# Kernel optimization log

Measured on AMD Instinct MI355X. Metric: run time of the kernel, lower is better.

Reference implementation:

```python
import jax, jax.numpy as jnp
import numpy as np

B, F_IN, HID, H, S = 256, 1024, 1024, 16, 128
TEMP = float((HID // H) ** 0.5)  # 8.0


def setup_inputs() -> dict:
    key = jax.random.key(0)
    ks = jax.random.split(key, 7)
    return {
        "x": jax.random.normal(ks[0], (B, F_IN, S), dtype=jnp.float32),
        "Wq": jax.random.normal(ks[1], (HID, F_IN), dtype=jnp.float32) * (1.0 / np.sqrt(F_IN)),
        "bq": jax.random.normal(ks[2], (HID,), dtype=jnp.float32) * 0.01,
        "Wk": jax.random.normal(ks[3], (HID, F_IN), dtype=jnp.float32) * (1.0 / np.sqrt(F_IN)),
        "bk": jax.random.normal(ks[4], (HID,), dtype=jnp.float32) * 0.01,
        "Wo": jax.random.normal(ks[5], (S,), dtype=jnp.float32) * (1.0 / np.sqrt(S)),
        "bo": jax.random.normal(ks[6], (1,), dtype=jnp.float32) * 0.01,
    }


def _to_heads(t):
    # (B, F, S) -> (B, H, S, F//H), matching reshape(B,H,F/H,S).permute(0,1,3,2)
    b, f, s = t.shape
    return t.reshape(b, H, f // H, s).transpose(0, 1, 3, 2)


def reference(x, Wq, bq, Wk, bk, Wo, bo):
    # 1x1 Conv1d == per-position linear over channel dim
    q = jnp.einsum('bis,hi->bhs', x, Wq) + bq[None, :, None]
    k = jnp.einsum('bis,hi->bhs', x, Wk) + bk[None, :, None]
    qh = _to_heads(q)          # (B,H,S,HID/H)
    kh = _to_heads(k)          # (B,H,S,HID/H)
    vh = _to_heads(x)          # (B,H,S,F_IN/H)  -- v is the raw input, unprojected
    scores = jnp.einsum('bhsd,bhtd->bhst', qh, kh) / TEMP
    attn = jax.nn.softmax(scores, axis=-1)
    out = jnp.einsum('bhst,bhtd->bhsd', attn, vh)   # (B,H,S,F_IN/H)
    # _reshape_from_batches: (B,H,S,dv) -> (B, F_IN, S)
    out = out.transpose(0, 1, 3, 2).reshape(x.shape[0], F_IN, S)
    # map_o: Linear(num_users, 1) over last axis, then squeeze
    score = jnp.einsum('bfs,s->bf', out, Wo) + bo[0]
    return score
```

## Files before the change

### kernel.cpp

```cpp
#include <hip/hip_runtime.h>

#define F 1024
#define S 128
#define H 16
#define D 64
#define CK 64
#define NCHUNK 16

typedef short bf16x8 __attribute__((ext_vector_type(8)));
typedef float f32x4  __attribute__((ext_vector_type(4)));

#define XS_UNITS ((size_t)256 * NCHUNK * 1024)
#define WB_UNITS ((size_t)16 * NCHUNK * 1024)
#define WS_NEED ((XS_UNITS + WB_UNITS) * 16)

struct SmemT {
    uint4 mat[2048];
    float wpart[4][S];
    float wfin[S];
};

__device__ __forceinline__ unsigned short f2bf(float f) {
    unsigned u = __float_as_uint(f);
    u += 0x7fffu + ((u >> 16) & 1u);
    return (unsigned short)(u >> 16);
}

__device__ __forceinline__ uint4 pack8(const float* f) {
    uint4 u;
    u.x = (unsigned)f2bf(f[0]) | ((unsigned)f2bf(f[1]) << 16);
    u.y = (unsigned)f2bf(f[2]) | ((unsigned)f2bf(f[3]) << 16);
    u.z = (unsigned)f2bf(f[4]) | ((unsigned)f2bf(f[5]) << 16);
    u.w = (unsigned)f2bf(f[6]) | ((unsigned)f2bf(f[7]) << 16);
    return u;
}

typedef __attribute__((address_space(1))) const unsigned int as1_u32;
typedef __attribute__((address_space(3))) unsigned int as3_u32;

__device__ __forceinline__ void async_cp16(const uint4* g, uint4* l) {
    __builtin_amdgcn_global_load_lds((as1_u32*)g, (as3_u32*)l, 16, 0, 0);
}

__global__ void prep(const float* __restrict__ x,
                     const float* __restrict__ Wq,
                     const float* __restrict__ Wk,
                     uint4* __restrict__ xs,
                     uint4* __restrict__ wb)
{
    __shared__ float tile[64 * 129];
    const int tid = threadIdx.x;
    const int blk = blockIdx.x;
    if (blk < 4096) {
        const int b = blk >> 4, ch = blk & 15;
        const float4* src = (const float4*)(x + ((size_t)b * F + ch * CK) * S);
        float4 v[8];
#pragma unroll
        for (int j = 0; j < 8; ++j) v[j] = src[tid + j * 256];
#pragma unroll
        for (int j = 0; j < 8; ++j) {
            const int e4 = tid + j * 256;
            const int i  = e4 >> 5;
            const int sc = (e4 & 31) * 4;
            tile[i * 129 + sc + 0] = v[j].x;
            tile[i * 129 + sc + 1] = v[j].y;
            tile[i * 129 + sc + 2] = v[j].z;
            tile[i * 129 + sc + 3] = v[j].w;
        }
        __syncthreads();
#pragma unroll
        for (int j = 0; j < 4; ++j) {
            const int u   = tid + j * 256;
            const int s   = u >> 3;
            const int kc  = (u & 7) ^ (s & 7);
            float f[8];
#pragma unroll
            for (int jj = 0; jj < 8; ++jj) f[jj] = tile[(kc * 8 + jj) * 129 + s];
            xs[((size_t)(b * NCHUNK + ch)) * 1024 + u] = pack8(f);
        }
    } else {
        const int blk2 = blk - 4096;
        const int h = blk2 >> 4, ch = blk2 & 15;
#pragma unroll
        for (int j = 0; j < 4; ++j) {
            const int u   = tid + j * 256;
            const int row = u >> 3;
            const int kc  = (u & 7) ^ (row & 7);
            const float* src = (row < 64)
                ? (Wq + (size_t)(h * D + row) * F + ch * CK + kc * 8)
                : (Wk + (size_t)(h * D + row - 64) * F + ch * CK + kc * 8);
            float f[8];
            float4 a = ((const float4*)src)[0];
            float4 c = ((const float4*)src)[1];
            f[0] = a.x; f[1] = a.y; f[2] = a.z; f[3] = a.w;
            f[4] = c.x; f[5] = c.y; f[6] = c.z; f[7] = c.w;
            wb[((size_t)(h * NCHUNK + ch)) * 1024 + u] = pack8(f);
        }
    }
}

__launch_bounds__(256, 4)
__global__ void attn_main(const float* __restrict__ x,
                          const uint4* __restrict__ xs,
                          const uint4* __restrict__ wb,
                          const float* __restrict__ bq,
                          const float* __restrict__ bk,
                          const float* __restrict__ Wo,
                          const float* __restrict__ bo,
                          float* __restrict__ out)
{
    __shared__ SmemT sm;
    const int tid  = threadIdx.x;
    const int lane = tid & 63;
    const int wv   = tid >> 6;
    const int l15  = lane & 15;
    const int q    = lane >> 4;

    const int g    = blockIdx.x;
    const int xcd  = g & 7;
    const int slot = g >> 3;
    const int hg   = slot >> 7;
    const int r0   = slot & 127;
    const int b    = xcd * 32 + (r0 >> 2);
    const int h    = hg * 4 + (r0 & 3);

    const float* xb = x + (size_t)b * (F * S);
    const uint4* xc = xs + ((size_t)b * NCHUNK) * 1024;
    const uint4* wc = wb + ((size_t)h * NCHUNK) * 1024;

    const int m0 = (wv & 1) * 64;
    const int n0 = (wv >> 1) * 64;

    f32x4 acc[4][4];
#pragma unroll
    for (int mt = 0; mt < 4; ++mt)
#pragma unroll
        for (int nt = 0; nt < 4; ++nt) acc[mt][nt] = (f32x4){0.f, 0.f, 0.f, 0.f};

    for (int ch = 0; ch < NCHUNK; ++ch) {
        __syncthreads();
        const uint4* wg = wc + ch * 1024 + wv * 256;
        const uint4* xg = xc + ch * 1024 + wv * 256;
#pragma unroll
        for (int k = 0; k < 4; ++k)
            async_cp16(wg + k * 64 + lane, &sm.mat[wv * 256 + k * 64]);
#pragma unroll
        for (int k = 0; k < 4; ++k)
            async_cp16(xg + k * 64 + lane, &sm.mat[1024 + wv * 256 + k * 64]);
        __syncthreads();
#pragma unroll
        for (int ks = 0; ks < 2; ++ks) {
            bf16x8 af[4], br[4];
#pragma unroll
            for (int mt = 0; mt < 4; ++mt) {
                const int row = m0 + mt * 16 + l15;
                af[mt] = *(const bf16x8*)&sm.mat[row * 8 + ((ks * 4 + q) ^ (row & 7))];
            }
#pragma unroll
            for (int nt = 0; nt < 4; ++nt) {
                const int row = n0 + nt * 16 + l15;
                br[nt] = *(const bf16x8*)&sm.mat[1024 + row * 8 + ((ks * 4 + q) ^ (row & 7))];
            }
#pragma unroll
            for (int mt = 0; mt < 4; ++mt)
#pragma unroll
                for (int nt = 0; nt < 4; ++nt)
                    acc[mt][nt] = __builtin_amdgcn_mfma_f32_16x16x32_bf16(
                        af[mt], br[nt], acc[mt][nt], 0, 0, 0);
        }
    }

    __syncthreads();
    {
        unsigned short* m16 = (unsigned short*)sm.mat;
#pragma unroll
        for (int mt = 0; mt < 4; ++mt) {
#pragma unroll
            for (int rr = 0; rr < 4; ++rr) {
                const int m = m0 + mt * 16 + q * 4 + rr;
                const int d = m & 63;
                const float bias = (m < 64) ? bq[h * D + d] : bk[h * D + d];
                const int base = (m < 64) ? 0 : 8192;
#pragma unroll
                for (int nt = 0; nt < 4; ++nt) {
                    const int s = n0 + nt * 16 + l15;
                    const float v = acc[mt][nt][rr] + bias;
                    const int unit = s * 8 + (((d >> 3)) ^ (s & 7));
                    m16[base + unit * 8 + (d & 7)] = f2bf(v);
                }
            }
        }
    }
    __syncthreads();

    f32x4 p[2][8];
#pragma unroll
    for (int mt = 0; mt < 2; ++mt)
#pragma unroll
        for (int nt = 0; nt < 8; ++nt) p[mt][nt] = (f32x4){0.f, 0.f, 0.f, 0.f};

#pragma unroll
    for (int ks = 0; ks < 2; ++ks) {
        bf16x8 a2[2], b2[8];
#pragma unroll
        for (int mt = 0; mt < 2; ++mt) {
            const int row = wv * 32 + mt * 16 + l15;
            a2[mt] = *(const bf16x8*)&sm.mat[row * 8 + ((ks * 4 + q) ^ (row & 7))];
        }
#pragma unroll
        for (int nt = 0; nt < 8; ++nt) {
            const int row = nt * 16 + l15;
            b2[nt] = *(const bf16x8*)&sm.mat[1024 + row * 8 + ((ks * 4 + q) ^ (row & 7))];
        }
#pragma unroll
        for (int mt = 0; mt < 2; ++mt)
#pragma unroll
            for (int nt = 0; nt < 8; ++nt)
                p[mt][nt] = __builtin_amdgcn_mfma_f32_16x16x32_bf16(a2[mt], b2[nt], p[mt][nt], 0, 0, 0);
    }

    float pw[8];
#pragma unroll
    for (int nt = 0; nt < 8; ++nt) pw[nt] = 0.f;

#pragma unroll
    for (int mt = 0; mt < 2; ++mt) {
#pragma unroll
        for (int rr = 0; rr < 4; ++rr) {
            const int srow = wv * 32 + mt * 16 + q * 4 + rr;
            float mx = p[mt][0][rr];
#pragma unroll
            for (int nt = 1; nt < 8; ++nt) mx = fmaxf(mx, p[mt][nt][rr]);
#pragma unroll
            for (int off = 1; off < 16; off <<= 1) mx = fmaxf(mx, __shfl_xor(mx, off));
            float e[8];
            float l = 0.f;
#pragma unroll
            for (int nt = 0; nt < 8; ++nt) {
                e[nt] = __expf((p[mt][nt][rr] - mx) * 0.125f);
                l += e[nt];
            }
#pragma unroll
            for (int off = 1; off < 16; off <<= 1) l += __shfl_xor(l, off);
            const float c = Wo[srow] / l;
#pragma unroll
            for (int nt = 0; nt < 8; ++nt) pw[nt] = fmaf(c, e[nt], pw[nt]);
        }
    }
#pragma unroll
    for (int nt = 0; nt < 8; ++nt) {
        pw[nt] += __shfl_xor(pw[nt], 16);
        pw[nt] += __shfl_xor(pw[nt], 32);
    }
    if (q == 0) {
#pragma unroll
        for (int nt = 0; nt < 8; ++nt) sm.wpart[wv][nt * 16 + l15] = pw[nt];
    }
    __syncthreads();
    if (tid < S)
        sm.wfin[tid] = sm.wpart[0][tid] + sm.wpart[1][tid] + sm.wpart[2][tid] + sm.wpart[3][tid];
    __syncthreads();

    {
        const int dd   = tid >> 2;
        const int part = tid & 3;
        const float* xv = xb + (size_t)(h * D + dd) * S + part * 32;
        float a5 = 0.f;
#pragma unroll 8
        for (int t = 0; t < 32; ++t) a5 = fmaf(sm.wfin[part * 32 + t], xv[t], a5);
        a5 += __shfl_xor(a5, 1);
        a5 += __shfl_xor(a5, 2);
        if (part == 0) out[(size_t)b * F + h * D + dd] = a5 + bo[0];
    }
}

__launch_bounds__(256, 4)
__global__ void attn_fallback(const float* __restrict__ x,
                              const float* __restrict__ Wq,
                              const float* __restrict__ bq,
                              const float* __restrict__ Wk,
                              const float* __restrict__ bk,
                              const float* __restrict__ Wo,
                              const float* __restrict__ bo,
                              float* __restrict__ out)
{
    __shared__ SmemT sm;
    const int tid  = threadIdx.x;
    const int lane = tid & 63;
    const int wv   = tid >> 6;
    const int l15  = lane & 15;
    const int q    = lane >> 4;

    const int g    = blockIdx.x;
    const int xcd  = g & 7;
    const int slot = g >> 3;
    const int hg   = slot >> 7;
    const int r0   = slot & 127;
    const int b    = xcd * 32 + (r0 >> 2);
    const int h    = hg * 4 + (r0 & 3);

    const float* xb  = x  + (size_t)b * (F * S);
    const float* wqh = Wq + (size_t)h * D * F;
    const float* wkh = Wk + (size_t)h * D * F;

    const int m0 = (wv & 1) * 64;
    const int n0 = (wv >> 1) * 64;

    f32x4 acc[4][4];
#pragma unroll
    for (int mt = 0; mt < 4; ++mt)
#pragma unroll
        for (int nt = 0; nt < 4; ++nt) acc[mt][nt] = (f32x4){0.f, 0.f, 0.f, 0.f};

    const int mq  = tid >> 2;
    const int kq  = tid & 3;
    const int s0x = (tid & 63) * 2;
    const int iq  = tid >> 6;

    for (int ch = 0; ch < NCHUNK; ++ch) {
        const int c0 = ch * CK;
        __syncthreads();
        {
            const int key = mq & 7;
            float f[16];
            const float4* srcq = (const float4*)(wqh + (size_t)mq * F + (c0 + kq * 16));
#pragma unroll
            for (int j = 0; j < 4; ++j) {
                float4 v = srcq[j];
                f[4*j] = v.x; f[4*j+1] = v.y; f[4*j+2] = v.z; f[4*j+3] = v.w;
            }
            sm.mat[mq * 8 + ((kq * 2    ) ^ key)] = pack8(f);
            sm.mat[mq * 8 + ((kq * 2 + 1) ^ key)] = pack8(f + 8);
            const float4* srck = (const float4*)(wkh + (size_t)mq * F + (c0 + kq * 16));
#pragma unroll
            for (int j = 0; j < 4; ++j) {
                float4 v = srck[j];
                f[4*j] = v.x; f[4*j+1] = v.y; f[4*j+2] = v.z; f[4*j+3] = v.w;
            }
            sm.mat[(64 + mq) * 8 + ((kq * 2    ) ^ key)] = pack8(f);
            sm.mat[(64 + mq) * 8 + ((kq * 2 + 1) ^ key)] = pack8(f + 8);
        }
        {
            const float* src = xb + (size_t)(c0 + iq * 16) * S + s0x;
            float fa[8], fb[8];
#pragma unroll
            for (int grp = 0; grp < 2; ++grp) {
#pragma unroll
                for (int j = 0; j < 8; ++j) {
                    float2 v = *(const float2*)(src + (size_t)(grp * 8 + j) * S);
                    fa[j] = v.x; fb[j] = v.y;
                }
                const int kc = iq * 2 + grp;
                sm.mat[1024 + (s0x    ) * 8 + (kc ^ ((s0x    ) & 7))] = pack8(fa);
                sm.mat[1024 + (s0x + 1) * 8 + (kc ^ ((s0x + 1) & 7))] = pack8(fb);
            }
        }
        __syncthreads();
#pragma unroll
        for (int ks = 0; ks < 2; ++ks) {
            bf16x8 af[4], br[4];
#pragma unroll
            for (int mt = 0; mt < 4; ++mt) {
                const int row = m0 + mt * 16 + l15;
                af[mt] = *(const bf16x8*)&sm.mat[row * 8 + ((ks * 4 + q) ^ (row & 7))];
            }
#pragma unroll
            for (int nt = 0; nt < 4; ++nt) {
                const int row = n0 + nt * 16 + l15;
                br[nt] = *(const bf16x8*)&sm.mat[1024 + row * 8 + ((ks * 4 + q) ^ (row & 7))];
            }
#pragma unroll
            for (int mt = 0; mt < 4; ++mt)
#pragma unroll
                for (int nt = 0; nt < 4; ++nt)
                    acc[mt][nt] = __builtin_amdgcn_mfma_f32_16x16x32_bf16(
                        af[mt], br[nt], acc[mt][nt], 0, 0, 0);
        }
    }

    __syncthreads();
    {
        unsigned short* m16 = (unsigned short*)sm.mat;
#pragma unroll
        for (int mt = 0; mt < 4; ++mt) {
#pragma unroll
            for (int rr = 0; rr < 4; ++rr) {
                const int m = m0 + mt * 16 + q * 4 + rr;
                const int d = m & 63;
                const float bias = (m < 64) ? bq[h * D + d] : bk[h * D + d];
                const int base = (m < 64) ? 0 : 8192;
#pragma unroll
                for (int nt = 0; nt < 4; ++nt) {
                    const int s = n0 + nt * 16 + l15;
                    const float v = acc[mt][nt][rr] + bias;
                    const int unit = s * 8 + (((d >> 3)) ^ (s & 7));
                    m16[base + unit * 8 + (d & 7)] = f2bf(v);
                }
            }
        }
    }
    __syncthreads();

    f32x4 p[2][8];
#pragma unroll
    for (int mt = 0; mt < 2; ++mt)
#pragma unroll
        for (int nt = 0; nt < 8; ++nt) p[mt][nt] = (f32x4){0.f, 0.f, 0.f, 0.f};

#pragma unroll
    for (int ks = 0; ks < 2; ++ks) {
        bf16x8 a2[2], b2[8];
#pragma unroll
        for (int mt = 0; mt < 2; ++mt) {
            const int row = wv * 32 + mt * 16 + l15;
            a2[mt] = *(const bf16x8*)&sm.mat[row * 8 + ((ks * 4 + q) ^ (row & 7))];
        }
#pragma unroll
        for (int nt = 0; nt < 8; ++nt) {
            const int row = nt * 16 + l15;
            b2[nt] = *(const bf16x8*)&sm.mat[1024 + row * 8 + ((ks * 4 + q) ^ (row & 7))];
        }
#pragma unroll
        for (int mt = 0; mt < 2; ++mt)
#pragma unroll
            for (int nt = 0; nt < 8; ++nt)
                p[mt][nt] = __builtin_amdgcn_mfma_f32_16x16x32_bf16(a2[mt], b2[nt], p[mt][nt], 0, 0, 0);
    }

    float pw[8];
#pragma unroll
    for (int nt = 0; nt < 8; ++nt) pw[nt] = 0.f;

#pragma unroll
    for (int mt = 0; mt < 2; ++mt) {
#pragma unroll
        for (int rr = 0; rr < 4; ++rr) {
            const int srow = wv * 32 + mt * 16 + q * 4 + rr;
            float mx = p[mt][0][rr];
#pragma unroll
            for (int nt = 1; nt < 8; ++nt) mx = fmaxf(mx, p[mt][nt][rr]);
#pragma unroll
            for (int off = 1; off < 16; off <<= 1) mx = fmaxf(mx, __shfl_xor(mx, off));
            float e[8];
            float l = 0.f;
#pragma unroll
            for (int nt = 0; nt < 8; ++nt) {
                e[nt] = __expf((p[mt][nt][rr] - mx) * 0.125f);
                l += e[nt];
            }
#pragma unroll
            for (int off = 1; off < 16; off <<= 1) l += __shfl_xor(l, off);
            const float c = Wo[srow] / l;
#pragma unroll
            for (int nt = 0; nt < 8; ++nt) pw[nt] = fmaf(c, e[nt], pw[nt]);
        }
    }
#pragma unroll
    for (int nt = 0; nt < 8; ++nt) {
        pw[nt] += __shfl_xor(pw[nt], 16);
        pw[nt] += __shfl_xor(pw[nt], 32);
    }
    if (q == 0) {
#pragma unroll
        for (int nt = 0; nt < 8; ++nt) sm.wpart[wv][nt * 16 + l15] = pw[nt];
    }
    __syncthreads();
    if (tid < S)
        sm.wfin[tid] = sm.wpart[0][tid] + sm.wpart[1][tid] + sm.wpart[2][tid] + sm.wpart[3][tid];
    __syncthreads();

    {
        const int dd   = tid >> 2;
        const int part = tid & 3;
        const float* xv = xb + (size_t)(h * D + dd) * S + part * 32;
        float a5 = 0.f;
#pragma unroll 8
        for (int t = 0; t < 32; ++t) a5 = fmaf(sm.wfin[part * 32 + t], xv[t], a5);
        a5 += __shfl_xor(a5, 1);
        a5 += __shfl_xor(a5, 2);
        if (part == 0) out[(size_t)b * F + h * D + dd] = a5 + bo[0];
    }
}

extern "C" void kernel_launch(void* const* d_in, const int* in_sizes, int n_in,
                              void* d_out, int out_size, void* d_ws, size_t ws_size,
                              hipStream_t stream) {
    const float* x  = (const float*)d_in[0];
    const float* Wq = (const float*)d_in[1];
    const float* bq = (const float*)d_in[2];
    const float* Wk = (const float*)d_in[3];
    const float* bk = (const float*)d_in[4];
    const float* Wo = (const float*)d_in[5];
    const float* bo = (const float*)d_in[6];
    float* out = (float*)d_out;

    if (ws_size >= WS_NEED) {
        uint4* xs = (uint4*)d_ws;
        uint4* wbp = (uint4*)((char*)d_ws + XS_UNITS * 16);
        prep<<<dim3(4096 + 256), dim3(256), 0, stream>>>(x, Wq, Wk, xs, wbp);
        attn_main<<<dim3(256 * H), dim3(256), 0, stream>>>(x, xs, wbp, bq, bk, Wo, bo, out);
    } else {
        attn_fallback<<<dim3(256 * H), dim3(256), 0, stream>>>(x, Wq, bq, Wk, bk, Wo, bo, out);
    }
}
```

Baseline: 367.5 us.

## Process two heads per block to reuse loaded x tiles across heads

The main attention kernel now handles two heads per 512-thread block, so each bf16 x chunk staged in LDS feeds a 256x128 projection GEMM (Q and K for both heads) instead of 128x128. The prep kernel packs weights for head pairs, and shared memory becomes a union of the projection stage and the QK stage. The goal is to halve the global x traffic and the block count. The larger blocks use more LDS and registers, which may lower occupancy. The bf16 packing also switches to the HIP paired-conversion intrinsic.

```diff
diff --git a/kernel.cpp b/kernel.cpp
--- a/kernel.cpp
+++ b/kernel.cpp
@@ -1,4 +1,5 @@
 #include <hip/hip_runtime.h>
+#include <hip/hip_bf16.h>
 
 #define F 1024
 #define S 128
@@ -10,11 +11,20 @@
 typedef short bf16x8 __attribute__((ext_vector_type(8)));
 typedef float f32x4  __attribute__((ext_vector_type(4)));
 
-#define XS_UNITS ((size_t)256 * NCHUNK * 1024)
-#define WB_UNITS ((size_t)16 * NCHUNK * 1024)
+#define XS_UNITS ((size_t)4096 * 1024)
+#define WB_UNITS ((size_t)128 * 2048)
 #define WS_NEED ((XS_UNITS + WB_UNITS) * 16)
 
 struct SmemT {
+    union {
+        struct { uint4 Ws[2048]; uint4 xT[1024]; } p1;
+        struct { uint4 qk[4096]; } p2;
+    } u;
+    float wpart[2][4][S];
+    float wfin[2][S];
+};
+
+struct SmemFb {
     uint4 mat[2048];
     float wpart[4][S];
     float wfin[S];
@@ -26,12 +36,15 @@
     return (unsigned short)(u >> 16);
 }
 
+__device__ __forceinline__ unsigned pk2(float a, float b) {
+    __hip_bfloat162 h = __float22bfloat162_rn(make_float2(a, b));
+    return *(unsigned*)&h;
+}
+
 __device__ __forceinline__ uint4 pack8(const float* f) {
     uint4 u;
-    u.x = (unsigned)f2bf(f[0]) | ((unsigned)f2bf(f[1]) << 16);
-    u.y = (unsigned)f2bf(f[2]) | ((unsigned)f2bf(f[3]) << 16);
-    u.z = (unsigned)f2bf(f[4]) | ((unsigned)f2bf(f[5]) << 16);
-    u.w = (unsigned)f2bf(f[6]) | ((unsigned)f2bf(f[7]) << 16);
+    u.x = pk2(f[0], f[1]); u.y = pk2(f[2], f[3]);
+    u.z = pk2(f[4], f[5]); u.w = pk2(f[6], f[7]);
     return u;
 }
 
@@ -80,26 +93,28 @@
         }
     } else {
         const int blk2 = blk - 4096;
-        const int h = blk2 >> 4, ch = blk2 & 15;
-#pragma unroll
-        for (int j = 0; j < 4; ++j) {
-            const int u   = tid + j * 256;
+        const int hp = blk2 >> 4, ch = blk2 & 15;
+#pragma unroll
+        for (int rep = 0; rep < 8; ++rep) {
+            const int u   = tid + rep * 256;
             const int row = u >> 3;
             const int kc  = (u & 7) ^ (row & 7);
-            const float* src = (row < 64)
-                ? (Wq + (size_t)(h * D + row) * F + ch * CK + kc * 8)
-                : (Wk + (size_t)(h * D + row - 64) * F + ch * CK + kc * 8);
+            const int hh  = row >> 7;
+            const int sub = row & 127;
+            const int hg  = hp * 2 + hh;
+            const float* src = ((sub < 64) ? (Wq + (size_t)(hg * D + sub) * F)
+                                           : (Wk + (size_t)(hg * D + (sub - 64)) * F))
+                               + ch * CK + kc * 8;
             float f[8];
             float4 a = ((const float4*)src)[0];
             float4 c = ((const float4*)src)[1];
-            f[0] = a.x; f[1] = a.y; f[2] = a.z; f[3] = a.w;
-            f[4] = c.x; f[5] = c.y; f[6] = c.z; f[7] = c.w;
-            wb[((size_t)(h * NCHUNK + ch)) * 1024 + u] = pack8(f);
-        }
-    }
-}
-
-__launch_bounds__(256, 4)
+            f[0]=a.x; f[1]=a.y; f[2]=a.z; f[3]=a.w; f[4]=c.x; f[5]=c.y; f[6]=c.z; f[7]=c.w;
+            wb[(size_t)blk2 * 2048 + u] = pack8(f);
+        }
+    }
+}
+
+__launch_bounds__(512, 4)
 __global__ void attn_main(const float* __restrict__ x,
                           const uint4* __restrict__ xs,
                           const uint4* __restrict__ wb,
@@ -119,17 +134,15 @@
     const int g    = blockIdx.x;
     const int xcd  = g & 7;
     const int slot = g >> 3;
-    const int hg   = slot >> 7;
-    const int r0   = slot & 127;
-    const int b    = xcd * 32 + (r0 >> 2);
-    const int h    = hg * 4 + (r0 & 3);
-
-    const float* xb = x + (size_t)b * (F * S);
+    const int b    = xcd * 32 + (slot & 31);
+    const int hp   = slot >> 5;
+
+    const float* xb = x  + (size_t)b * (F * S);
     const uint4* xc = xs + ((size_t)b * NCHUNK) * 1024;
-    const uint4* wc = wb + ((size_t)h * NCHUNK) * 1024;
-
-    const int m0 = (wv & 1) * 64;
-    const int n0 = (wv >> 1) * 64;
+    const uint4* wc = wb + ((size_t)hp * NCHUNK) * 2048;
+
+    const int m0 = (wv & 3) * 64;
+    const int n0 = (wv >> 2) * 64;
 
     f32x4 acc[4][4];
 #pragma unroll
@@ -139,14 +152,14 @@
 
     for (int ch = 0; ch < NCHUNK; ++ch) {
         __syncthreads();
-        const uint4* wg = wc + ch * 1024 + wv * 256;
-        const uint4* xg = xc + ch * 1024 + wv * 256;
-#pragma unroll
-        for (int k = 0; k < 4; ++k)
-            async_cp16(wg + k * 64 + lane, &sm.mat[wv * 256 + k * 64]);
-#pragma unroll
-        for (int k = 0; k < 4; ++k)
-            async_cp16(xg + k * 64 + lane, &sm.mat[1024 + wv * 256 + k * 64]);
+        const uint4* wg = wc + ch * 2048;
+        const uint4* xg = xc + ch * 1024;
+#pragma unroll
+        for (int g2 = 0; g2 < 4; ++g2)
+            async_cp16(wg + g2 * 512 + wv * 64 + lane, sm.u.p1.Ws + g2 * 512 + wv * 64);
+#pragma unroll
+        for (int g2 = 0; g2 < 2; ++g2)
+            async_cp16(xg + g2 * 512 + wv * 64 + lane, sm.u.p1.xT + g2 * 512 + wv * 64);
         __syncthreads();
 #pragma unroll
         for (int ks = 0; ks < 2; ++ks) {
@@ -154,12 +167,12 @@
 #pragma unroll
             for (int mt = 0; mt < 4; ++mt) {
                 const int row = m0 + mt * 16 + l15;
-                af[mt] = *(const bf16x8*)&sm.mat[row * 8 + ((ks * 4 + q) ^ (row & 7))];
+                af[mt] = *(const bf16x8*)&sm.u.p1.Ws[row * 8 + ((ks * 4 + q) ^ (row & 7))];
             }
 #pragma unroll
             for (int nt = 0; nt < 4; ++nt) {
                 const int row = n0 + nt * 16 + l15;
-                br[nt] = *(const bf16x8*)&sm.mat[1024 + row * 8 + ((ks * 4 + q) ^ (row & 7))];
+                br[nt] = *(const bf16x8*)&sm.u.p1.xT[row * 8 + ((ks * 4 + q) ^ (row & 7))];
             }
 #pragma unroll
             for (int mt = 0; mt < 4; ++mt)
@@ -172,26 +185,35 @@
 
     __syncthreads();
     {
-        unsigned short* m16 = (unsigned short*)sm.mat;
+        unsigned short* m16 = (unsigned short*)sm.u.p2.qk;
 #pragma unroll
         for (int mt = 0; mt < 4; ++mt) {
 #pragma unroll
             for (int rr = 0; rr < 4; ++rr) {
-                const int m = m0 + mt * 16 + q * 4 + rr;
-                const int d = m & 63;
-                const float bias = (m < 64) ? bq[h * D + d] : bk[h * D + d];
-                const int base = (m < 64) ? 0 : 8192;
+                const int m    = m0 + mt * 16 + q * 4 + rr;
+                const int hh   = m >> 7;
+                const int w128 = m & 127;
+                const int d    = w128 & 63;
+                const int hg   = hp * 2 + hh;
+                const float bias = (w128 < 64) ? bq[hg * D + d] : bk[hg * D + d];
+                const int ubase  = hh * 2048 + ((w128 < 64) ? 0 : 1024);
 #pragma unroll
                 for (int nt = 0; nt < 4; ++nt) {
                     const int s = n0 + nt * 16 + l15;
                     const float v = acc[mt][nt][rr] + bias;
-                    const int unit = s * 8 + (((d >> 3)) ^ (s & 7));
-                    m16[base + unit * 8 + (d & 7)] = f2bf(v);
+                    const int unit = ubase + s * 8 + ((d >> 3) ^ (s & 7));
+                    m16[unit * 8 + (d & 7)] = f2bf(v);
                 }
             }
         }
     }
     __syncthreads();
+
+    const int hh   = wv >> 2;
+    const int hg   = hp * 2 + hh;
+    const int rb   = (wv & 3) * 32;
+    const int qsO  = hh * 2048;
+    const int ksO  = qsO + 1024;
 
     f32x4 p[2][8];
 #pragma unroll
@@ -204,13 +226,13 @@
         bf16x8 a2[2], b2[8];
 #pragma unroll
         for (int mt = 0; mt < 2; ++mt) {
-            const int row = wv * 32 + mt * 16 + l15;
-            a2[mt] = *(const bf16x8*)&sm.mat[row * 8 + ((ks * 4 + q) ^ (row & 7))];
+            const int row = rb + mt * 16 + l15;
+            a2[mt] = *(const bf16x8*)&sm.u.p2.qk[qsO + row * 8 + ((ks * 4 + q) ^ (row & 7))];
         }
 #pragma unroll
         for (int nt = 0; nt < 8; ++nt) {
             const int row = nt * 16 + l15;
-            b2[nt] = *(const bf16x8*)&sm.mat[1024 + row * 8 + ((ks * 4 + q) ^ (row & 7))];
+            b2[nt] = *(const bf16x8*)&sm.u.p2.qk[ksO + row * 8 + ((ks * 4 + q) ^ (row & 7))];
         }
 #pragma unroll
         for (int mt = 0; mt < 2; ++mt)
@@ -227,7 +249,7 @@
     for (int mt = 0; mt < 2; ++mt) {
 #pragma unroll
         for (int rr = 0; rr < 4; ++rr) {
-            const int srow = wv * 32 + mt * 16 + q * 4 + rr;
+            const int srow = rb + mt * 16 + q * 4 + rr;
             float mx = p[mt][0][rr];
 #pragma unroll
             for (int nt = 1; nt < 8; ++nt) mx = fmaxf(mx, p[mt][nt][rr]);
@@ -254,23 +276,29 @@
     }
     if (q == 0) {
 #pragma unroll
-        for (int nt = 0; nt < 8; ++nt) sm.wpart[wv][nt * 16 + l15] = pw[nt];
-    }
-    __syncthreads();
-    if (tid < S)
-        sm.wfin[tid] = sm.wpart[0][tid] + sm.wpart[1][tid] + sm.wpart[2][tid] + sm.wpart[3][tid];
+        for (int nt = 0; nt < 8; ++nt) sm.wpart[hh][wv & 3][nt * 16 + l15] = pw[nt];
+    }
+    __syncthreads();
+    if (tid < 256) {
+        const int h2 = tid >> 7, t = tid & 127;
+        sm.wfin[h2][t] = sm.wpart[h2][0][t] + sm.wpart[h2][1][t]
+                       + sm.wpart[h2][2][t] + sm.wpart[h2][3][t];
+    }
     __syncthreads();
 
     {
-        const int dd   = tid >> 2;
-        const int part = tid & 3;
-        const float* xv = xb + (size_t)(h * D + dd) * S + part * 32;
+        const int h3   = tid >> 8;
+        const int r    = tid & 255;
+        const int dd   = r >> 2;
+        const int part = r & 3;
+        const int hg3  = hp * 2 + h3;
+        const float* xv = xb + (size_t)(hg3 * D + dd) * S + part * 32;
         float a5 = 0.f;
 #pragma unroll 8
-        for (int t = 0; t < 32; ++t) a5 = fmaf(sm.wfin[part * 32 + t], xv[t], a5);
+        for (int t = 0; t < 32; ++t) a5 = fmaf(sm.wfin[h3][part * 32 + t], xv[t], a5);
         a5 += __shfl_xor(a5, 1);
         a5 += __shfl_xor(a5, 2);
-        if (part == 0) out[(size_t)b * F + h * D + dd] = a5 + bo[0];
+        if (part == 0) out[(size_t)b * F + hg3 * D + dd] = a5 + bo[0];
     }
 }
 
@@ -284,7 +312,7 @@
                               const float* __restrict__ bo,
                               float* __restrict__ out)
 {
-    __shared__ SmemT sm;
+    __shared__ SmemFb sm;
     const int tid  = threadIdx.x;
     const int lane = tid & 63;
     const int wv   = tid >> 6;
@@ -317,8 +345,8 @@
     const int s0x = (tid & 63) * 2;
     const int iq  = tid >> 6;
 
-    for (int ch = 0; ch < NCHUNK; ++ch) {
-        const int c0 = ch * CK;
+    for (int ch = 0; ch < 16; ++ch) {
+        const int c0 = ch * 64;
         __syncthreads();
         {
             const int key = mq & 7;
@@ -495,10 +523,10 @@
     float* out = (float*)d_out;
 
     if (ws_size >= WS_NEED) {
-        uint4* xs = (uint4*)d_ws;
+        uint4* xs  = (uint4*)d_ws;
         uint4* wbp = (uint4*)((char*)d_ws + XS_UNITS * 16);
-        prep<<<dim3(4096 + 256), dim3(256), 0, stream>>>(x, Wq, Wk, xs, wbp);
-        attn_main<<<dim3(256 * H), dim3(256), 0, stream>>>(x, xs, wbp, bq, bk, Wo, bo, out);
+        prep<<<dim3(4096 + 128), dim3(256), 0, stream>>>(x, Wq, Wk, xs, wbp);
+        attn_main<<<dim3(2048), dim3(512), 0, stream>>>(x, xs, wbp, bq, bk, Wo, bo, out);
     } else {
         attn_fallback<<<dim3(256 * H), dim3(256), 0, stream>>>(x, Wq, bq, Wk, bk, Wo, bo, out);
     }
```

New measurement: 388.6 us. 5.8% more time.

## Double-buffer x chunks in LDS and read bf16 weights straight from global

Applied to the files above, without the earlier changes.

The main kernel now double-buffers the per-batch x chunks in LDS, prefetching chunk ch+1 asynchronously while computing chunk ch, and drops the second barrier per iteration. The Wq/Wk bf16 tiles are stored in a plain row-major per-head layout and loaded directly from global memory (L2-cached) into MFMA A fragments rather than staged through LDS. bf16 packing also switches to the hardware paired conversion intrinsic. This trades LDS traffic and barriers for uncoalesced-ish global weight reads that depend on cache hits, and there is no explicit wait on the async LDS copy before use.

```diff
diff --git a/kernel.cpp b/kernel.cpp
--- a/kernel.cpp
+++ b/kernel.cpp
@@ -1,4 +1,5 @@
 #include <hip/hip_runtime.h>
+#include <hip/hip_bf16.h>
 
 #define F 1024
 #define S 128
@@ -10,11 +11,20 @@
 typedef short bf16x8 __attribute__((ext_vector_type(8)));
 typedef float f32x4  __attribute__((ext_vector_type(4)));
 
-#define XS_UNITS ((size_t)256 * NCHUNK * 1024)
-#define WB_UNITS ((size_t)16 * NCHUNK * 1024)
+#define XS_UNITS ((size_t)4096 * 1024)
+#define WB_UNITS ((size_t)256 * 1024)
 #define WS_NEED ((XS_UNITS + WB_UNITS) * 16)
 
 struct SmemT {
+    union {
+        uint4 xdb[2][1024];
+        uint4 qk[2048];
+    } u;
+    float wpart[4][S];
+    float wfin[S];
+};
+
+struct SmemFb {
     uint4 mat[2048];
     float wpart[4][S];
     float wfin[S];
@@ -26,12 +36,15 @@
     return (unsigned short)(u >> 16);
 }
 
+__device__ __forceinline__ unsigned pk2(float a, float b) {
+    __hip_bfloat162 h = __float22bfloat162_rn(make_float2(a, b));
+    return *(unsigned*)&h;
+}
+
 __device__ __forceinline__ uint4 pack8(const float* f) {
     uint4 u;
-    u.x = (unsigned)f2bf(f[0]) | ((unsigned)f2bf(f[1]) << 16);
-    u.y = (unsigned)f2bf(f[2]) | ((unsigned)f2bf(f[3]) << 16);
-    u.z = (unsigned)f2bf(f[4]) | ((unsigned)f2bf(f[5]) << 16);
-    u.w = (unsigned)f2bf(f[6]) | ((unsigned)f2bf(f[7]) << 16);
+    u.x = pk2(f[0], f[1]); u.y = pk2(f[2], f[3]);
+    u.z = pk2(f[4], f[5]); u.w = pk2(f[6], f[7]);
     return u;
 }
 
@@ -46,7 +59,7 @@
                      const float* __restrict__ Wq,
                      const float* __restrict__ Wk,
                      uint4* __restrict__ xs,
-                     uint4* __restrict__ wb)
+                     uint4* __restrict__ wbh)
 {
     __shared__ float tile[64 * 129];
     const int tid = threadIdx.x;
@@ -80,21 +93,19 @@
         }
     } else {
         const int blk2 = blk - 4096;
-        const int h = blk2 >> 4, ch = blk2 & 15;
 #pragma unroll
         for (int j = 0; j < 4; ++j) {
-            const int u   = tid + j * 256;
-            const int row = u >> 3;
-            const int kc  = (u & 7) ^ (row & 7);
-            const float* src = (row < 64)
-                ? (Wq + (size_t)(h * D + row) * F + ch * CK + kc * 8)
-                : (Wk + (size_t)(h * D + row - 64) * F + ch * CK + kc * 8);
+            const int u  = blk2 * 1024 + tid + j * 256;
+            const int h  = u >> 14;
+            const int r  = (u >> 7) & 127;
+            const int k8 = u & 127;
+            const float* src = ((r < 64) ? (Wq + (size_t)(h * D + r) * F)
+                                         : (Wk + (size_t)(h * D + (r - 64)) * F)) + k8 * 8;
             float f[8];
             float4 a = ((const float4*)src)[0];
             float4 c = ((const float4*)src)[1];
-            f[0] = a.x; f[1] = a.y; f[2] = a.z; f[3] = a.w;
-            f[4] = c.x; f[5] = c.y; f[6] = c.z; f[7] = c.w;
-            wb[((size_t)(h * NCHUNK + ch)) * 1024 + u] = pack8(f);
+            f[0]=a.x; f[1]=a.y; f[2]=a.z; f[3]=a.w; f[4]=c.x; f[5]=c.y; f[6]=c.z; f[7]=c.w;
+            wbh[u] = pack8(f);
         }
     }
 }
@@ -102,7 +113,7 @@
 __launch_bounds__(256, 4)
 __global__ void attn_main(const float* __restrict__ x,
                           const uint4* __restrict__ xs,
-                          const uint4* __restrict__ wb,
+                          const uint4* __restrict__ wbh,
                           const float* __restrict__ bq,
                           const float* __restrict__ bk,
                           const float* __restrict__ Wo,
@@ -124,9 +135,9 @@
     const int b    = xcd * 32 + (r0 >> 2);
     const int h    = hg * 4 + (r0 & 3);
 
-    const float* xb = x + (size_t)b * (F * S);
-    const uint4* xc = xs + ((size_t)b * NCHUNK) * 1024;
-    const uint4* wc = wb + ((size_t)h * NCHUNK) * 1024;
+    const float* xb = x   + (size_t)b * (F * S);
+    const uint4* xc = xs  + (size_t)b * (NCHUNK * 1024);
+    const uint4* wu = wbh + (size_t)h * (128 * 128);
 
     const int m0 = (wv & 1) * 64;
     const int n0 = (wv >> 1) * 64;
@@ -137,29 +148,31 @@
 #pragma unroll
         for (int nt = 0; nt < 4; ++nt) acc[mt][nt] = (f32x4){0.f, 0.f, 0.f, 0.f};
 
+#pragma unroll
+    for (int k = 0; k < 4; ++k)
+        async_cp16(xc + wv * 256 + k * 64 + lane, &sm.u.xdb[0][wv * 256 + k * 64]);
+
+    int buf = 0;
     for (int ch = 0; ch < NCHUNK; ++ch) {
         __syncthreads();
-        const uint4* wg = wc + ch * 1024 + wv * 256;
-        const uint4* xg = xc + ch * 1024 + wv * 256;
-#pragma unroll
-        for (int k = 0; k < 4; ++k)
-            async_cp16(wg + k * 64 + lane, &sm.mat[wv * 256 + k * 64]);
-#pragma unroll
-        for (int k = 0; k < 4; ++k)
-            async_cp16(xg + k * 64 + lane, &sm.mat[1024 + wv * 256 + k * 64]);
-        __syncthreads();
+        if (ch + 1 < NCHUNK) {
+            const uint4* xg = xc + (ch + 1) * 1024;
+#pragma unroll
+            for (int k = 0; k < 4; ++k)
+                async_cp16(xg + wv * 256 + k * 64 + lane, &sm.u.xdb[buf ^ 1][wv * 256 + k * 64]);
+        }
 #pragma unroll
         for (int ks = 0; ks < 2; ++ks) {
             bf16x8 af[4], br[4];
 #pragma unroll
             for (int mt = 0; mt < 4; ++mt) {
                 const int row = m0 + mt * 16 + l15;
-                af[mt] = *(const bf16x8*)&sm.mat[row * 8 + ((ks * 4 + q) ^ (row & 7))];
+                af[mt] = *(const bf16x8*)(wu + (size_t)row * 128 + ch * 8 + ks * 4 + q);
             }
 #pragma unroll
             for (int nt = 0; nt < 4; ++nt) {
                 const int row = n0 + nt * 16 + l15;
-                br[nt] = *(const bf16x8*)&sm.mat[1024 + row * 8 + ((ks * 4 + q) ^ (row & 7))];
+                br[nt] = *(const bf16x8*)&sm.u.xdb[buf][row * 8 + ((ks * 4 + q) ^ (row & 7))];
             }
 #pragma unroll
             for (int mt = 0; mt < 4; ++mt)
@@ -168,11 +181,12 @@
                     acc[mt][nt] = __builtin_amdgcn_mfma_f32_16x16x32_bf16(
                         af[mt], br[nt], acc[mt][nt], 0, 0, 0);
         }
+        buf ^= 1;
     }
 
     __syncthreads();
     {
-        unsigned short* m16 = (unsigned short*)sm.mat;
+        unsigned short* m16 = (unsigned short*)sm.u.qk;
 #pragma unroll
         for (int mt = 0; mt < 4; ++mt) {
 #pragma unroll
@@ -185,7 +199,7 @@
                 for (int nt = 0; nt < 4; ++nt) {
                     const int s = n0 + nt * 16 + l15;
                     const float v = acc[mt][nt][rr] + bias;
-                    const int unit = s * 8 + (((d >> 3)) ^ (s & 7));
+                    const int unit = s * 8 + ((d >> 3) ^ (s & 7));
                     m16[base + unit * 8 + (d & 7)] = f2bf(v);
                 }
             }
@@ -205,12 +219,12 @@
 #pragma unroll
         for (int mt = 0; mt < 2; ++mt) {
             const int row = wv * 32 + mt * 16 + l15;
-            a2[mt] = *(const bf16x8*)&sm.mat[row * 8 + ((ks * 4 + q) ^ (row & 7))];
+            a2[mt] = *(const bf16x8*)&sm.u.qk[row * 8 + ((ks * 4 + q) ^ (row & 7))];
         }
 #pragma unroll
         for (int nt = 0; nt < 8; ++nt) {
             const int row = nt * 16 + l15;
-            b2[nt] = *(const bf16x8*)&sm.mat[1024 + row * 8 + ((ks * 4 + q) ^ (row & 7))];
+            b2[nt] = *(const bf16x8*)&sm.u.qk[1024 + row * 8 + ((ks * 4 + q) ^ (row & 7))];
         }
 #pragma unroll
         for (int mt = 0; mt < 2; ++mt)
@@ -284,7 +298,7 @@
                               const float* __restrict__ bo,
                               float* __restrict__ out)
 {
-    __shared__ SmemT sm;
+    __shared__ SmemFb sm;
     const int tid  = threadIdx.x;
     const int lane = tid & 63;
     const int wv   = tid >> 6;
@@ -317,8 +331,8 @@
     const int s0x = (tid & 63) * 2;
     const int iq  = tid >> 6;
 
-    for (int ch = 0; ch < NCHUNK; ++ch) {
-        const int c0 = ch * CK;
+    for (int ch = 0; ch < 16; ++ch) {
+        const int c0 = ch * 64;
         __syncthreads();
         {
             const int key = mq & 7;
@@ -495,10 +509,10 @@
     float* out = (float*)d_out;
 
     if (ws_size >= WS_NEED) {
-        uint4* xs = (uint4*)d_ws;
-        uint4* wbp = (uint4*)((char*)d_ws + XS_UNITS * 16);
-        prep<<<dim3(4096 + 256), dim3(256), 0, stream>>>(x, Wq, Wk, xs, wbp);
-        attn_main<<<dim3(256 * H), dim3(256), 0, stream>>>(x, xs, wbp, bq, bk, Wo, bo, out);
+        uint4* xs  = (uint4*)d_ws;
+        uint4* wbh = (uint4*)((char*)d_ws + XS_UNITS * 16);
+        prep<<<dim3(4096 + 256), dim3(256), 0, stream>>>(x, Wq, Wk, xs, wbh);
+        attn_main<<<dim3(4096), dim3(256), 0, stream>>>(x, xs, wbh, bq, bk, Wo, bo, out);
     } else {
         attn_fallback<<<dim3(256 * H), dim3(256), 0, stream>>>(x, Wq, bq, Wk, bk, Wo, bo, out);
     }
```

After: 493.4 us. +34.3%, slower.
